# Performance work log

Hardware: AMD Instinct MI355X
Metric: run time of the kernel (lower is better)

The kernel has to match this reference:

```python
import jax, jax.numpy as jnp
import numpy as np

B, C_IN, C_OUT, H, F_DIM = 32, 64, 1, 4096, 8
OUT_CH, K = F_DIM + 1, F_DIM // 2 + 1          # even-feature branch: 9 channels, kernel (1,5)
HALF = F_DIM * (F_DIM + 1) // 2                # 36 upper-triangular entries
MIN_VEC = 0.001
IU = np.triu_indices(F_DIM)                    # torch.triu_indices(f, f)


def setup_inputs() -> dict:
    key = jax.random.key(0)
    k1, k2, k3, k4, k5 = jax.random.split(key, 5)
    x = jax.random.normal(k1, (B, C_IN, H, F_DIM), jnp.float32)
    w_n = jax.random.normal(k2, (C_OUT, C_IN, 1, 1), jnp.float32) * 0.05
    b_n = jax.random.normal(k3, (C_OUT,), jnp.float32) * 0.05
    w_p = jax.random.normal(k4, (OUT_CH, C_IN, 1, K), jnp.float32) * 0.05
    b_p = jax.random.normal(k5, (OUT_CH,), jnp.float32) * 0.05
    return {"x": x, "w_n": w_n, "b_n": b_n, "w_p": w_p, "b_p": b_p}


def _forward(x, w_n, b_n, w_p, b_p):
    # n_conv: 1x1 conv -> softplus  (loc: [B, C_OUT, H, F_DIM])
    loc = jax.nn.softplus(
        jnp.einsum('bchw,oc->bohw', x, w_n[:, :, 0, 0]) + b_n[None, :, None, None])
    # p_conv: (1,K) valid conv -> softplus  (scale: [B, OUT_CH, H, W_out])
    p = jax.lax.conv_general_dilated(
        x, w_p, window_strides=(1, 1), padding='VALID',
        dimension_numbers=('NCHW', 'OIHW', 'NCHW')) + b_p[None, :, None, None]
    scale = jax.nn.softplus(p)
    # unsqueeze(1) + permute(0,1,3,2,4) + flatten(start_dim=3) -> [B,1,H,HALF]
    sigma = jnp.transpose(scale, (0, 2, 1, 3)).reshape(B, 1, H, HALF)
    # scatter upper-tri values symmetrically into [B,1,H,F,F]
    z = jnp.zeros((B, 1, H, F_DIM, F_DIM), sigma.dtype)
    z = z.at[..., IU[0], IU[1]].set(sigma)
    z = z.at[..., IU[1], IU[0]].set(sigma)
    # batched eigh, clamp eigenvalues, reconstruct PD matrix, symmetrize
    eigval, eigvec = jnp.linalg.eigh(z)
    clamped = jnp.maximum(eigval, MIN_VEC)
    pd = jnp.einsum('...ij,...j,...kj->...ik', eigvec, clamped, eigvec)
    pd = 0.5 * (pd + jnp.swapaxes(pd, -1, -2))
    return loc, pd


def reference(x, w_n, b_n, w_p, b_p):
    return _forward(x, w_n, b_n, w_p, b_p)
```

## Files before the change

kernel.cpp:

```cpp
#include <hip/hip_runtime.h>
#include <math.h>

#define B_      32
#define C_IN    64
#define H_      4096
#define F_      8
#define OUT_CH  9
#define KW      5
#define BH      (B_ * H_)
#define LOC_N   (BH * F_)
#define NSWEEP  6
#define MIN_VEC 0.001f

__device__ const int PAIRS[7][4][2] = {
  {{0,7},{1,6},{2,5},{3,4}},
  {{0,6},{5,7},{1,4},{2,3}},
  {{0,5},{4,6},{3,7},{1,2}},
  {{0,4},{3,5},{2,6},{1,7}},
  {{0,3},{2,4},{1,5},{6,7}},
  {{0,2},{1,3},{4,7},{5,6}},
  {{0,1},{2,7},{3,6},{4,5}},
};

#define SYM(i,j) (((i) < (j)) ? A[i][j] : A[j][i])

__device__ __forceinline__ float softplus_f(float v) {
    return fmaxf(v, 0.0f) + __logf(1.0f + __expf(-fabsf(v)));
}

__global__ __launch_bounds__(256, 2)
void mgauss_fused(const float* __restrict__ x,
                  const float* __restrict__ w_n,
                  const float* __restrict__ b_n,
                  const float* __restrict__ w_p,
                  const float* __restrict__ b_p,
                  float* __restrict__ out)
{
    const int t = blockIdx.x * 256 + threadIdx.x;
    const int b = t >> 12;
    const int h = t & 4095;

    const float* xp = x + ((size_t)b * C_IN * H_ + h) * F_;

    float la[F_];
    #pragma unroll
    for (int w = 0; w < F_; ++w) la[w] = 0.0f;
    float pa[OUT_CH][4];
    #pragma unroll
    for (int o = 0; o < OUT_CH; ++o)
        #pragma unroll
        for (int wo = 0; wo < 4; ++wo) pa[o][wo] = 0.0f;

    #pragma unroll 4
    for (int c = 0; c < C_IN; ++c) {
        const float4 x0 = *(const float4*)(xp + (size_t)c * (H_ * F_));
        const float4 x1 = *(const float4*)(xp + (size_t)c * (H_ * F_) + 4);
        const float xa[F_] = {x0.x, x0.y, x0.z, x0.w, x1.x, x1.y, x1.z, x1.w};

        const float wn = w_n[c];
        #pragma unroll
        for (int w = 0; w < F_; ++w) la[w] = fmaf(xa[w], wn, la[w]);

        #pragma unroll
        for (int o = 0; o < OUT_CH; ++o) {
            #pragma unroll
            for (int k = 0; k < KW; ++k) {
                const float wv = w_p[(o * C_IN + c) * KW + k];
                #pragma unroll
                for (int wo = 0; wo < 4; ++wo)
                    pa[o][wo] = fmaf(xa[wo + k], wv, pa[o][wo]);
            }
        }
    }

    {
        const float bn = b_n[0];
        float lv[F_];
        #pragma unroll
        for (int w = 0; w < F_; ++w) lv[w] = softplus_f(la[w] + bn);
        float* lo = out + (size_t)t * F_;
        *(float4*)(lo)     = make_float4(lv[0], lv[1], lv[2], lv[3]);
        *(float4*)(lo + 4) = make_float4(lv[4], lv[5], lv[6], lv[7]);
    }

    float A[F_][F_];
    {
        float sig[36];
        #pragma unroll
        for (int o = 0; o < OUT_CH; ++o) {
            const float bp = b_p[o];
            #pragma unroll
            for (int wo = 0; wo < 4; ++wo)
                sig[o * 4 + wo] = softplus_f(pa[o][wo] + bp);
        }
        int k = 0;
        #pragma unroll
        for (int i = 0; i < F_; ++i)
            #pragma unroll
            for (int j = i; j < F_; ++j) {
                A[i][j] = sig[k];
                ++k;
            }
    }

    float V[F_][F_];
    #pragma unroll
    for (int i = 0; i < F_; ++i)
        #pragma unroll
        for (int j = 0; j < F_; ++j)
            V[i][j] = (i == j) ? 1.0f : 0.0f;

    for (int sweep = 0; sweep < NSWEEP; ++sweep) {
        #pragma unroll
        for (int r = 0; r < 7; ++r) {
            float cs[4], sn[4], tv[4];
            #pragma unroll
            for (int j = 0; j < 4; ++j) {
                const int p = PAIRS[r][j][0], q = PAIRS[r][j][1];
                const float apq = A[p][q];
                const float app = A[p][p];
                const float aqq = A[q][q];
                float th = (aqq - app) / (2.0f * apq);
                float tt = 1.0f / (fabsf(th) + sqrtf(fmaf(th, th, 1.0f)));
                tt = (th < 0.0f) ? -tt : tt;
                tt = (apq == 0.0f) ? 0.0f : tt;
                const float cc = 1.0f / sqrtf(fmaf(tt, tt, 1.0f));
                cs[j] = cc; sn[j] = tt * cc; tv[j] = tt;
            }
            #pragma unroll
            for (int j = 0; j < 4; ++j) {
                const int p = PAIRS[r][j][0], q = PAIRS[r][j][1];
                const float cc = cs[j], ss = sn[j], tt = tv[j];
                const float apq = A[p][q];
                A[p][p] = fmaf(-tt, apq, A[p][p]);
                A[q][q] = fmaf( tt, apq, A[q][q]);
                A[p][q] = 0.0f;
                #pragma unroll
                for (int i = 0; i < F_; ++i) {
                    if (i == p || i == q) continue;
                    const float aip = SYM(i, p);
                    const float aiq = SYM(i, q);
                    SYM(i, p) = fmaf(-ss, aiq, cc * aip);
                    SYM(i, q) = fmaf( ss, aip, cc * aiq);
                }
            }
            #pragma unroll
            for (int j = 0; j < 4; ++j) {
                const int p = PAIRS[r][j][0], q = PAIRS[r][j][1];
                const float cc = cs[j], ss = sn[j];
                #pragma unroll
                for (int i = 0; i < F_; ++i) {
                    const float u = V[i][p], v = V[i][q];
                    V[i][p] = fmaf(-ss, v, cc * u);
                    V[i][q] = fmaf( ss, u, cc * v);
                }
            }
        }
    }

    float lam[F_];
    #pragma unroll
    for (int k = 0; k < F_; ++k) lam[k] = fmaxf(A[k][k], MIN_VEC);

    float W[F_][F_];
    #pragma unroll
    for (int i = 0; i < F_; ++i)
        #pragma unroll
        for (int k = 0; k < F_; ++k)
            W[i][k] = V[i][k] * lam[k];

    float PD[F_][F_];
    #pragma unroll
    for (int i = 0; i < F_; ++i) {
        #pragma unroll
        for (int j = i; j < F_; ++j) {
            float acc = 0.0f;
            #pragma unroll
            for (int k = 0; k < F_; ++k)
                acc = fmaf(W[i][k], V[j][k], acc);
            PD[i][j] = acc;
            PD[j][i] = acc;
        }
    }

    float* po = out + LOC_N + (size_t)t * (F_ * F_);
    #pragma unroll
    for (int i = 0; i < F_; ++i) {
        *(float4*)(po + i * F_)     = make_float4(PD[i][0], PD[i][1], PD[i][2], PD[i][3]);
        *(float4*)(po + i * F_ + 4) = make_float4(PD[i][4], PD[i][5], PD[i][6], PD[i][7]);
    }
}

extern "C" void kernel_launch(void* const* d_in, const int* in_sizes, int n_in,
                              void* d_out, int out_size, void* d_ws, size_t ws_size,
                              hipStream_t stream) {
    const float* x   = (const float*)d_in[0];
    const float* w_n = (const float*)d_in[1];
    const float* b_n = (const float*)d_in[2];
    const float* w_p = (const float*)d_in[3];
    const float* b_p = (const float*)d_in[4];
    float* out = (float*)d_out;

    dim3 grid(BH / 256);
    dim3 block(256);
    hipLaunchKernelGGL(mgauss_fused, grid, block, 0, stream,
                       x, w_n, b_n, w_p, b_p, out);
}
```

Baseline: 457.7 us.

## Split channel reduction across two thread halves and use fast rcp/rsq intrinsics

Each block now handles 128 positions with 256 threads. The two halves each reduce 32 of the 64 input channels, then combine their partial sums through shared memory. Both halves run the Jacobi eigensolve redundantly, and each writes half of the PD rows. The launch bound is raised to 4 blocks per SM and the divisions and sqrt are replaced with hardware rcp/sqrt/rsq intrinsics. The aim is more parallelism and occupancy in the memory-bound conv phase, at the cost of doubling the eigensolver work and adding extra register pressure and synchronization.

```diff
diff --git a/kernel.cpp b/kernel.cpp
--- a/kernel.cpp
+++ b/kernel.cpp
@@ -28,7 +28,7 @@
     return fmaxf(v, 0.0f) + __logf(1.0f + __expf(-fabsf(v)));
 }
 
-__global__ __launch_bounds__(256, 2)
+__global__ __launch_bounds__(256, 4)
 void mgauss_fused(const float* __restrict__ x,
                   const float* __restrict__ w_n,
                   const float* __restrict__ b_n,
@@ -36,48 +36,69 @@
                   const float* __restrict__ b_p,
                   float* __restrict__ out)
 {
-    const int t = blockIdx.x * 256 + threadIdx.x;
-    const int b = t >> 12;
-    const int h = t & 4095;
+    __shared__ float xsh[128][45];
+
+    const int tid  = threadIdx.x;
+    const int wv   = tid >> 6;
+    const int lane = tid & 63;
+    const int halfsel = wv >> 1;
+    const int pl   = ((wv & 1) << 6) | lane;
+    const int t    = blockIdx.x * 128 + pl;
+    const int b    = t >> 12;
+    const int h    = t & 4095;
 
     const float* xp = x + ((size_t)b * C_IN * H_ + h) * F_;
-
-    float la[F_];
-    #pragma unroll
-    for (int w = 0; w < F_; ++w) la[w] = 0.0f;
-    float pa[OUT_CH][4];
-    #pragma unroll
-    for (int o = 0; o < OUT_CH; ++o)
-        #pragma unroll
-        for (int wo = 0; wo < 4; ++wo) pa[o][wo] = 0.0f;
+    const int c0 = __builtin_amdgcn_readfirstlane(halfsel << 5);
+
+    float acc[44];
+    #pragma unroll
+    for (int k = 0; k < 44; ++k) acc[k] = 0.0f;
 
     #pragma unroll 4
-    for (int c = 0; c < C_IN; ++c) {
-        const float4 x0 = *(const float4*)(xp + (size_t)c * (H_ * F_));
-        const float4 x1 = *(const float4*)(xp + (size_t)c * (H_ * F_) + 4);
+    for (int c = 0; c < 32; ++c) {
+        const int cc = c0 + c;
+        const float4 x0 = *(const float4*)(xp + (size_t)cc * (H_ * F_));
+        const float4 x1 = *(const float4*)(xp + (size_t)cc * (H_ * F_) + 4);
         const float xa[F_] = {x0.x, x0.y, x0.z, x0.w, x1.x, x1.y, x1.z, x1.w};
 
-        const float wn = w_n[c];
-        #pragma unroll
-        for (int w = 0; w < F_; ++w) la[w] = fmaf(xa[w], wn, la[w]);
+        const float wn = w_n[cc];
+        #pragma unroll
+        for (int w = 0; w < F_; ++w) acc[w] = fmaf(xa[w], wn, acc[w]);
 
         #pragma unroll
         for (int o = 0; o < OUT_CH; ++o) {
             #pragma unroll
             for (int k = 0; k < KW; ++k) {
-                const float wv = w_p[(o * C_IN + c) * KW + k];
+                const float wvp = w_p[(o * C_IN + cc) * KW + k];
                 #pragma unroll
                 for (int wo = 0; wo < 4; ++wo)
-                    pa[o][wo] = fmaf(xa[wo + k], wv, pa[o][wo]);
-            }
-        }
-    }
-
-    {
+                    acc[8 + o * 4 + wo] = fmaf(xa[wo + k], wvp, acc[8 + o * 4 + wo]);
+            }
+        }
+    }
+
+    if (halfsel) {
+        #pragma unroll
+        for (int k = 0; k < 44; ++k) xsh[pl][k] = acc[k];
+    }
+    __syncthreads();
+    if (!halfsel) {
+        #pragma unroll
+        for (int k = 0; k < 44; ++k) acc[k] += xsh[pl][k];
+        #pragma unroll
+        for (int k = 8; k < 44; ++k) xsh[pl][k] = acc[k];
+    }
+    __syncthreads();
+    if (halfsel) {
+        #pragma unroll
+        for (int k = 8; k < 44; ++k) acc[k] = xsh[pl][k];
+    }
+
+    if (!halfsel) {
         const float bn = b_n[0];
         float lv[F_];
         #pragma unroll
-        for (int w = 0; w < F_; ++w) lv[w] = softplus_f(la[w] + bn);
+        for (int w = 0; w < F_; ++w) lv[w] = softplus_f(acc[w] + bn);
         float* lo = out + (size_t)t * F_;
         *(float4*)(lo)     = make_float4(lv[0], lv[1], lv[2], lv[3]);
         *(float4*)(lo + 4) = make_float4(lv[4], lv[5], lv[6], lv[7]);
@@ -91,7 +112,7 @@
             const float bp = b_p[o];
             #pragma unroll
             for (int wo = 0; wo < 4; ++wo)
-                sig[o * 4 + wo] = softplus_f(pa[o][wo] + bp);
+                sig[o * 4 + wo] = softplus_f(acc[8 + o * 4 + wo] + bp);
         }
         int k = 0;
         #pragma unroll
@@ -120,11 +141,12 @@
                 const float apq = A[p][q];
                 const float app = A[p][p];
                 const float aqq = A[q][q];
-                float th = (aqq - app) / (2.0f * apq);
-                float tt = 1.0f / (fabsf(th) + sqrtf(fmaf(th, th, 1.0f)));
+                const float th = (aqq - app) * 0.5f * __builtin_amdgcn_rcpf(apq);
+                float tt = __builtin_amdgcn_rcpf(fabsf(th) +
+                              __builtin_amdgcn_sqrtf(fmaf(th, th, 1.0f)));
                 tt = (th < 0.0f) ? -tt : tt;
                 tt = (apq == 0.0f) ? 0.0f : tt;
-                const float cc = 1.0f / sqrtf(fmaf(tt, tt, 1.0f));
+                const float cc = __builtin_amdgcn_rsqf(fmaf(tt, tt, 1.0f));
                 cs[j] = cc; sn[j] = tt * cc; tv[j] = tt;
             }
             #pragma unroll
@@ -174,20 +196,28 @@
     for (int i = 0; i < F_; ++i) {
         #pragma unroll
         for (int j = i; j < F_; ++j) {
-            float acc = 0.0f;
+            float fa = 0.0f;
             #pragma unroll
             for (int k = 0; k < F_; ++k)
-                acc = fmaf(W[i][k], V[j][k], acc);
-            PD[i][j] = acc;
-            PD[j][i] = acc;
+                fa = fmaf(W[i][k], V[j][k], fa);
+            PD[i][j] = fa;
+            PD[j][i] = fa;
         }
     }
 
     float* po = out + LOC_N + (size_t)t * (F_ * F_);
-    #pragma unroll
-    for (int i = 0; i < F_; ++i) {
-        *(float4*)(po + i * F_)     = make_float4(PD[i][0], PD[i][1], PD[i][2], PD[i][3]);
-        *(float4*)(po + i * F_ + 4) = make_float4(PD[i][4], PD[i][5], PD[i][6], PD[i][7]);
+    if (!halfsel) {
+        #pragma unroll
+        for (int i = 0; i < 4; ++i) {
+            *(float4*)(po + i * F_)     = make_float4(PD[i][0], PD[i][1], PD[i][2], PD[i][3]);
+            *(float4*)(po + i * F_ + 4) = make_float4(PD[i][4], PD[i][5], PD[i][6], PD[i][7]);
+        }
+    } else {
+        #pragma unroll
+        for (int i = 4; i < 8; ++i) {
+            *(float4*)(po + i * F_)     = make_float4(PD[i][0], PD[i][1], PD[i][2], PD[i][3]);
+            *(float4*)(po + i * F_ + 4) = make_float4(PD[i][4], PD[i][5], PD[i][6], PD[i][7]);
+        }
     }
 }
 
@@ -201,7 +231,7 @@
     const float* b_p = (const float*)d_in[4];
     float* out = (float*)d_out;
 
-    dim3 grid(BH / 256);
+    dim3 grid(BH / 128);
     dim3 block(256);
     hipLaunchKernelGGL(mgauss_fused, grid, block, 0, stream,
                        x, w_n, b_n, w_p, b_p, out);
```

After: 1.233 ms. 2.69x slower.
